# Kernel tuning notes

Hardware: AMD Instinct MI355X
Metric: run time of the kernel (lower is better)

Reference implementation:

```python
import jax, jax.numpy as jnp
import numpy as np

B, S, D, R = 4, 4096, 1024, 64


def setup_inputs() -> dict:
    key = jax.random.key(0)
    k1, k2 = jax.random.split(key)
    x = jax.random.normal(k1, (B, S, D), dtype=jnp.float32)
    # nn.init.uniform_(proj, -0.05, 0.05)
    proj = jax.random.uniform(k2, (D, R), dtype=jnp.float32, minval=-0.05, maxval=0.05)
    return {"x": x, "proj": proj}


def reference(x, proj):
    # Low-rank projection: [B, S, D] @ [D, R] -> [B, S, R]
    p = jnp.matmul(x, proj)
    # Pairwise squared L2 distances via ||a||^2 + ||b||^2 - 2 a.b
    # (algebraically equal to the broadcasted (a-b)^2 sum in the original)
    sq = jnp.sum(p * p, axis=-1)                      # [B, S]
    cross = jnp.einsum("bsr,btr->bst", p, p)          # [B, S, S]
    dist = sq[:, :, None] + sq[:, None, :] - 2.0 * cross
    return jnp.maximum(dist, 0.0)
```

## Files before the change

kernel.cpp:

```cpp
#include <hip/hip_runtime.h>
#include <hip/hip_bf16.h>

#define M_TOT 16384
#define DK    1024
#define RN    64
#define SQ_S  4096

typedef __attribute__((ext_vector_type(8))) short  short8;
typedef __attribute__((ext_vector_type(4))) float  f32x4;

__device__ __forceinline__ unsigned short f2bf(float f) {
    unsigned u = __float_as_uint(f);
    return (unsigned short)((u + 0x7fffu + ((u >> 16) & 1u)) >> 16);
}
__device__ __forceinline__ float bf2f(unsigned short h) {
    return __uint_as_float((unsigned)h << 16);
}

__global__ __launch_bounds__(256) void prep_kernel(
        const float* __restrict__ proj,
        unsigned short* __restrict__ pTh,
        unsigned short* __restrict__ pTl) {
    int idx = blockIdx.x * 256 + threadIdx.x;
    int r = idx >> 10;
    int k = idx & 1023;
    float v = proj[k * RN + r];
    unsigned short hi = f2bf(v);
    pTh[idx] = hi;
    pTl[idx] = f2bf(v - bf2f(hi));
}

__global__ __launch_bounds__(256) void phase1_kernel(
        const float* __restrict__ x,
        const unsigned short* __restrict__ pTh,
        const unsigned short* __restrict__ pTl,
        unsigned short* __restrict__ p_hi,
        unsigned short* __restrict__ p_lo,
        float* __restrict__ sq) {
    const int tid  = threadIdx.x;
    const int wave = tid >> 6;
    const int lane = tid & 63;
    const int lr   = lane & 15;
    const int lg   = lane >> 4;

    const long m0    = (long)blockIdx.x * 16;
    const int  kbase = wave * 256;
    const float* xrow = x + (m0 + lr) * DK + kbase + lg * 8;

    f32x4 acc[4] = {f32x4{0,0,0,0}, f32x4{0,0,0,0}, f32x4{0,0,0,0}, f32x4{0,0,0,0}};

    #pragma unroll 2
    for (int kc = 0; kc < 8; ++kc) {
        f32x4 a0 = *(const f32x4*)(xrow + kc * 32);
        f32x4 a1 = *(const f32x4*)(xrow + kc * 32 + 4);
        short8 ah, al;
        #pragma unroll
        for (int i = 0; i < 4; ++i) {
            unsigned short h0 = f2bf(a0[i]);
            ah[i] = (short)h0;
            al[i] = (short)f2bf(a0[i] - bf2f(h0));
            unsigned short h1 = f2bf(a1[i]);
            ah[i + 4] = (short)h1;
            al[i + 4] = (short)f2bf(a1[i] - bf2f(h1));
        }
        #pragma unroll
        for (int cj = 0; cj < 4; ++cj) {
            long bo = (long)(cj * 16 + lr) * DK + kbase + kc * 32 + lg * 8;
            short8 bh = *(const short8*)(pTh + bo);
            short8 bl = *(const short8*)(pTl + bo);
            f32x4 c = acc[cj];
            c = __builtin_amdgcn_mfma_f32_16x16x32_bf16(ah, bh, c, 0, 0, 0);
            c = __builtin_amdgcn_mfma_f32_16x16x32_bf16(ah, bl, c, 0, 0, 0);
            c = __builtin_amdgcn_mfma_f32_16x16x32_bf16(al, bh, c, 0, 0, 0);
            acc[cj] = c;
        }
    }

    __shared__ float red[4][64][17];
    #pragma unroll
    for (int cj = 0; cj < 4; ++cj)
        #pragma unroll
        for (int j = 0; j < 4; ++j)
            red[wave][lane][cj * 4 + j] = acc[cj][j];
    __syncthreads();

    if (wave == 0) {
        #pragma unroll
        for (int j = 0; j < 4; ++j) {
            const long m = m0 + lg * 4 + j;
            float ssum = 0.f;
            #pragma unroll
            for (int cj = 0; cj < 4; ++cj) {
                const int sl = cj * 4 + j;
                float v = red[0][lane][sl] + red[1][lane][sl]
                        + red[2][lane][sl] + red[3][lane][sl];
                unsigned short hi = f2bf(v);
                p_hi[m * RN + cj * 16 + lr] = hi;
                p_lo[m * RN + cj * 16 + lr] = f2bf(v - bf2f(hi));
                ssum += v * v;
            }
            ssum += __shfl_xor(ssum, 1);
            ssum += __shfl_xor(ssum, 2);
            ssum += __shfl_xor(ssum, 4);
            ssum += __shfl_xor(ssum, 8);
            if (lr == 0) sq[m] = ssum;
        }
    }
}

__global__ __launch_bounds__(256) void phase2_kernel(
        const unsigned short* __restrict__ p_hi,
        const unsigned short* __restrict__ p_lo,
        const float* __restrict__ sq,
        float* __restrict__ out) {
    const int b  = blockIdx.z;
    const long s0 = (long)blockIdx.y * 128;
    const long t0 = (long)blockIdx.x * 128;
    const int tid  = threadIdx.x;
    const int wave = tid >> 6;
    const int lane = tid & 63;
    const int ws = wave >> 1, wt = wave & 1;
    const int lr = lane & 15, lg = lane >> 4;

    const unsigned short* ph  = p_hi + (long)b * SQ_S * RN;
    const unsigned short* pl  = p_lo + (long)b * SQ_S * RN;
    const float*          sqb = sq   + (long)b * SQ_S;

    f32x4 acc[4][4];
    #pragma unroll
    for (int i = 0; i < 4; ++i)
        #pragma unroll
        for (int j = 0; j < 4; ++j) acc[i][j] = f32x4{0, 0, 0, 0};

    const long trow = t0 + wt * 64 + lr;
    const long srow = s0 + ws * 64 + lr;

    #pragma unroll
    for (int kc = 0; kc < 2; ++kc) {
        short8 th_[4], tl_[4], sh_[4], sl_[4];
        #pragma unroll
        for (int i = 0; i < 4; ++i) {
            long ao = (trow + i * 16) * RN + kc * 32 + lg * 8;
            th_[i] = *(const short8*)(ph + ao);
            tl_[i] = *(const short8*)(pl + ao);
            long bo = (srow + i * 16) * RN + kc * 32 + lg * 8;
            sh_[i] = *(const short8*)(ph + bo);
            sl_[i] = *(const short8*)(pl + bo);
        }
        #pragma unroll
        for (int ai = 0; ai < 4; ++ai)
            #pragma unroll
            for (int bj = 0; bj < 4; ++bj) {
                f32x4 c = acc[ai][bj];
                c = __builtin_amdgcn_mfma_f32_16x16x32_bf16(th_[ai], sh_[bj], c, 0, 0, 0);
                c = __builtin_amdgcn_mfma_f32_16x16x32_bf16(th_[ai], sl_[bj], c, 0, 0, 0);
                c = __builtin_amdgcn_mfma_f32_16x16x32_bf16(tl_[ai], sh_[bj], c, 0, 0, 0);
                acc[ai][bj] = c;
            }
    }

    f32x4 sqt[4];
    #pragma unroll
    for (int ai = 0; ai < 4; ++ai)
        sqt[ai] = *(const f32x4*)(sqb + t0 + wt * 64 + ai * 16 + lg * 4);
    float sqs[4];
    #pragma unroll
    for (int bj = 0; bj < 4; ++bj)
        sqs[bj] = sqb[s0 + ws * 64 + bj * 16 + lr];

    float* outb = out + (long)b * SQ_S * SQ_S;
    #pragma unroll
    for (int bj = 0; bj < 4; ++bj) {
        const long s = s0 + ws * 64 + bj * 16 + lr;
        float* orow = outb + s * SQ_S + t0 + wt * 64;
        #pragma unroll
        for (int ai = 0; ai < 4; ++ai) {
            f32x4 v;
            #pragma unroll
            for (int j = 0; j < 4; ++j)
                v[j] = fmaxf(sqs[bj] + sqt[ai][j] - 2.0f * acc[ai][bj][j], 0.0f);
            __builtin_nontemporal_store(v, (f32x4*)(orow + ai * 16 + lg * 4));
        }
    }
}

extern "C" void kernel_launch(void* const* d_in, const int* in_sizes, int n_in,
                              void* d_out, int out_size, void* d_ws, size_t ws_size,
                              hipStream_t stream) {
    const float* x    = (const float*)d_in[0];
    const float* proj = (const float*)d_in[1];
    float* out = (float*)d_out;

    unsigned short* pTh  = (unsigned short*)d_ws;
    unsigned short* pTl  = pTh + RN * DK;
    unsigned short* p_hi = pTl + RN * DK;
    unsigned short* p_lo = p_hi + (long)M_TOT * RN;
    float*          sqp  = (float*)(p_lo + (long)M_TOT * RN);

    prep_kernel<<<(RN * DK) / 256, 256, 0, stream>>>(proj, pTh, pTl);
    phase1_kernel<<<M_TOT / 16, 256, 0, stream>>>(x, pTh, pTl, p_hi, p_lo, sqp);
    phase2_kernel<<<dim3(SQ_S / 128, SQ_S / 128, 4), 256, 0, stream>>>(p_hi, p_lo, sqp, out);
}
```

Baseline: 374.2 us.

## Remap phase2 grid across XCDs, use 8-wave blocks, switch to regular stores

Phase 2 now launches a 1-D grid of 512-thread blocks. The block index is permuted so neighbouring tiles are distributed across XCD chiplets. Each wave computes a 32x64 sub-tile instead of 64x64, which lowers the accumulator register count and may raise occupancy. Nontemporal output stores are replaced with normal stores, which may change cache behaviour for the large output write.

After: 405.1 us. 1.08x slower.

```diff
diff --git a/kernel.cpp b/kernel.cpp
--- a/kernel.cpp
+++ b/kernel.cpp
@@ -108,49 +108,57 @@
     }
 }
 
-__global__ __launch_bounds__(256) void phase2_kernel(
+__global__ __launch_bounds__(512) void phase2_kernel(
         const unsigned short* __restrict__ p_hi,
         const unsigned short* __restrict__ p_lo,
         const float* __restrict__ sq,
         float* __restrict__ out) {
-    const int b  = blockIdx.z;
-    const long s0 = (long)blockIdx.y * 128;
-    const long t0 = (long)blockIdx.x * 128;
+    const int wg = (blockIdx.x & 7) * 512 + (blockIdx.x >> 3);
+    const int b      = wg >> 10;
+    const int r      = wg & 1023;
+    const long s0 = (long)(r >> 5) * 128;
+    const long t0 = (long)(r & 31) * 128;
+
     const int tid  = threadIdx.x;
     const int wave = tid >> 6;
     const int lane = tid & 63;
-    const int ws = wave >> 1, wt = wave & 1;
+    const int sstrip = wave >> 1;
+    const int thalf  = wave & 1;
     const int lr = lane & 15, lg = lane >> 4;
 
     const unsigned short* ph  = p_hi + (long)b * SQ_S * RN;
     const unsigned short* pl  = p_lo + (long)b * SQ_S * RN;
     const float*          sqb = sq   + (long)b * SQ_S;
 
-    f32x4 acc[4][4];
-    #pragma unroll
-    for (int i = 0; i < 4; ++i)
-        #pragma unroll
-        for (int j = 0; j < 4; ++j) acc[i][j] = f32x4{0, 0, 0, 0};
-
-    const long trow = t0 + wt * 64 + lr;
-    const long srow = s0 + ws * 64 + lr;
+    f32x4 acc[4][2];
+    #pragma unroll
+    for (int i = 0; i < 4; ++i) {
+        acc[i][0] = f32x4{0, 0, 0, 0};
+        acc[i][1] = f32x4{0, 0, 0, 0};
+    }
+
+    const long tbase = t0 + thalf * 64;
+    const long sbase = s0 + sstrip * 32;
 
     #pragma unroll
     for (int kc = 0; kc < 2; ++kc) {
-        short8 th_[4], tl_[4], sh_[4], sl_[4];
+        short8 th_[4], tl_[4], sh_[2], sl_[2];
         #pragma unroll
         for (int i = 0; i < 4; ++i) {
-            long ao = (trow + i * 16) * RN + kc * 32 + lg * 8;
+            long ao = (tbase + i * 16 + lr) * RN + kc * 32 + lg * 8;
             th_[i] = *(const short8*)(ph + ao);
             tl_[i] = *(const short8*)(pl + ao);
-            long bo = (srow + i * 16) * RN + kc * 32 + lg * 8;
+        }
+        #pragma unroll
+        for (int i = 0; i < 2; ++i) {
+            long bo = (sbase + i * 16 + lr) * RN + kc * 32 + lg * 8;
             sh_[i] = *(const short8*)(ph + bo);
             sl_[i] = *(const short8*)(pl + bo);
         }
         #pragma unroll
         for (int ai = 0; ai < 4; ++ai)
             #pragma unroll
-            for (int bj = 0; bj < 4; ++bj) {
+            for (int bj = 0; bj < 2; ++bj) {
                 f32x4 c = acc[ai][bj];
                 c = __builtin_amdgcn_mfma_f32_16x16x32_bf16(th_[ai], sh_[bj], c, 0, 0, 0);
                 c = __builtin_amdgcn_mfma_f32_16x16x32_bf16(th_[ai], sl_[bj], c, 0, 0, 0);
@@ -162,24 +170,21 @@
     f32x4 sqt[4];
     #pragma unroll
     for (int ai = 0; ai < 4; ++ai)
-        sqt[ai] = *(const f32x4*)(sqb + t0 + wt * 64 + ai * 16 + lg * 4);
-    float sqs[4];
-    #pragma unroll
-    for (int bj = 0; bj < 4; ++bj)
-        sqs[bj] = sqb[s0 + ws * 64 + bj * 16 + lr];
+        sqt[ai] = *(const f32x4*)(sqb + tbase + ai * 16 + lg * 4);
 
     float* outb = out + (long)b * SQ_S * SQ_S;
     #pragma unroll
-    for (int bj = 0; bj < 4; ++bj) {
-        const long s = s0 + ws * 64 + bj * 16 + lr;
-        float* orow = outb + s * SQ_S + t0 + wt * 64;
+    for (int bj = 0; bj < 2; ++bj) {
+        const long s = sbase + bj * 16 + lr;
+        const float sqs = sqb[s];
+        float* orow = outb + s * SQ_S + tbase;
         #pragma unroll
         for (int ai = 0; ai < 4; ++ai) {
             f32x4 v;
             #pragma unroll
             for (int j = 0; j < 4; ++j)
-                v[j] = fmaxf(sqs[bj] + sqt[ai][j] - 2.0f * acc[ai][bj][j], 0.0f);
-            __builtin_nontemporal_store(v, (f32x4*)(orow + ai * 16 + lg * 4));
+                v[j] = fmaxf(sqs + sqt[ai][j] - 2.0f * acc[ai][bj][j], 0.0f);
+            *(f32x4*)(orow + ai * 16 + lg * 4) = v;
         }
     }
 }
@@ -199,5 +204,5 @@
 
     prep_kernel<<<(RN * DK) / 256, 256, 0, stream>>>(proj, pTh, pTl);
     phase1_kernel<<<M_TOT / 16, 256, 0, stream>>>(x, pTh, pTl, p_hi, p_lo, sqp);
-    phase2_kernel<<<dim3(SQ_S / 128, SQ_S / 128, 4), 256, 0, stream>>>(p_hi, p_lo, sqp, out);
-}
+    phase2_kernel<<<dim3(4096), 512, 0, stream>>>(p_hi, p_lo, sqp, out);
+}
```
